# Optimization experiments

Measured on AMD Instinct MI355X. Metric: run time of the kernel, lower is better.

The kernel has to match this reference:

```python
import jax, jax.numpy as jnp
import numpy as np

TEMP = 0.1
EPS = 1e-12  # F.normalize eps


def setup_inputs() -> dict:
    key = jax.random.key(0)
    k1, k2 = jax.random.split(key)
    B, C, N = 8, 128, 4096
    features = jax.random.normal(k1, (B, C, N), dtype=jnp.float32)
    labels_all = jax.random.randint(k2, (B, N), 0, 16, dtype=jnp.int32)
    return {"features": features, "labels_all": labels_all}


def _per_cloud_loss(features_map, labels):
    # features_map: [C, N], labels: [N]
    v = features_map.T  # [N, C]
    v = v / jnp.maximum(jnp.linalg.norm(v, axis=1, keepdims=True), EPS)
    dp = jnp.exp(jnp.matmul(v, v.T) / TEMP)  # [N, N]
    n = dp.shape[0]
    # remove diagonal (dot_products - diag(diagonal))
    dp = dp * (1.0 - jnp.eye(n, dtype=dp.dtype))
    mask = labels[:, None] == labels[None, :]  # [N, N]
    positives = jnp.sum(jnp.where(mask, dp, 0.0), axis=1)
    negatives = jnp.sum(jnp.where(mask, 0.0, dp), axis=1)
    deviation = -jnp.log(positives / (positives + negatives))
    return jnp.mean(deviation)


def reference(features, labels_all):
    # features: [B, C, N], labels_all: [B, N]
    losses = jax.vmap(_per_cloud_loss)(features, labels_all)  # [B]
    return jnp.mean(losses)
```

## Files before the change

kernel.cpp:

```cpp
#include <hip/hip_runtime.h>
#include <hip/hip_bf16.h>
#include <math.h>

#define BATCH 8
#define NPTS 4096
#define CH 128
#define TILE 128

#define SQRT_TEMP_LOG2E 3.79828256f

typedef __attribute__((ext_vector_type(4))) float f32x4;
typedef __attribute__((ext_vector_type(4))) int   i32x4;
typedef __attribute__((ext_vector_type(8))) short bf16x8;

typedef __attribute__((address_space(3))) unsigned int lds_uint;
typedef __attribute__((address_space(1))) const unsigned int gbl_uint;

__device__ __forceinline__ void load_lds16(const void* g, const void* l) {
    __builtin_amdgcn_global_load_lds((gbl_uint*)g, (lds_uint*)l, 16, 0, 0);
}

__device__ __forceinline__ float fast_exp2(float x) {
    return __builtin_amdgcn_exp2f(x);
}

__global__ __launch_bounds__(256) void normalize_kernel(
    const float* __restrict__ f, __hip_bfloat16* __restrict__ vn,
    float* __restrict__ pos, float* __restrict__ neg)
{
    int idx = blockIdx.x * 256 + threadIdx.x;
    int point = idx >> 2, q = idx & 3;
    int b = point >> 12, n = point & (NPTS - 1);
    const float* base = f + (size_t)b * CH * NPTS + (size_t)(q * 32) * NPTS + n;

    float x[32];
    float ss = 0.0f;
    #pragma unroll
    for (int c = 0; c < 32; c++) {
        x[c] = base[(size_t)c * NPTS];
        ss += x[c] * x[c];
    }
    ss += __shfl_xor(ss, 1);
    ss += __shfl_xor(ss, 2);
    float scale = SQRT_TEMP_LOG2E / fmaxf(sqrtf(ss), 1e-12f);

    __hip_bfloat16* out = vn + (size_t)point * CH + q * 32;
    #pragma unroll
    for (int c0 = 0; c0 < 32; c0 += 8) {
        union { __hip_bfloat16 h[8]; uint4 u; } pk;
        #pragma unroll
        for (int j = 0; j < 8; j++)
            pk.h[j] = __float2bfloat16(x[c0 + j] * scale);
        *((uint4*)(out + c0)) = pk.u;
    }
    if (q == 0) pos[point] = 0.0f;
    else if (q == 1) neg[point] = 0.0f;
}

__global__ __launch_bounds__(512, 6) void tile_kernel(
    const __hip_bfloat16* __restrict__ vn, const int* __restrict__ labels,
    float* __restrict__ pos, float* __restrict__ neg)
{
    __shared__ short lB[TILE * CH];
    __shared__ int labC[TILE];

    const int b  = blockIdx.z;
    const int rt = blockIdx.y, ct = blockIdx.x;
    const bool diag = (rt == ct);

    const int tid = threadIdx.x;
    const int w = tid >> 6, lane = tid & 63;
    const int lane15 = lane & 15, quad = lane >> 4;

    const int row0 = rt * TILE, col0 = ct * TILE;
    const __hip_bfloat16* vb = vn + (size_t)b * NPTS * CH;

    if (tid < 128) labC[tid] = labels[b * NPTS + col0 + tid];

    {
        const __hip_bfloat16* Bb = vb + (size_t)col0 * CH;
        #pragma unroll
        for (int i = 0; i < 4; i++) {
            int rsw = (i * 4 + quad) & 15;
            int g   = lane15 ^ rsw;
            int row = w * 16 + i * 4 + quad;
            int ldsrow = w * 16 + i * 4;
            load_lds16(Bb + (size_t)row * CH + g * 8, &lB[ldsrow * CH]);
        }
    }

    const int rowi = w * 16 + lane15;
    bf16x8 afrag[4];
    {
        const __hip_bfloat16* Arow = vb + (size_t)(row0 + rowi) * CH;
        #pragma unroll
        for (int ks = 0; ks < 4; ks++)
            afrag[ks] = *(const bf16x8*)(Arow + (ks * 4 + quad) * 8);
    }
    const int lr = labels[b * NPTS + row0 + rowi];

    __syncthreads();

    f32x4 acc[8] = {};
    #pragma unroll
    for (int ks = 0; ks < 4; ks++) {
        int chunk = ((ks * 4 + quad) ^ lane15) << 3;
        #pragma unroll
        for (int ni = 0; ni < 8; ni++) {
            bf16x8 bfrag = *(const bf16x8*)&lB[(ni * 16 + lane15) * CH + chunk];
            acc[ni] = __builtin_amdgcn_mfma_f32_16x16x32_bf16(
                bfrag, afrag[ks], acc[ni], 0, 0, 0);
        }
    }

    float p = 0.0f, tt = 0.0f;
    if (diag) {
        #pragma unroll
        for (int ni = 0; ni < 8; ni++) {
            const i32x4 lc = *(const i32x4*)&labC[ni * 16 + quad * 4];
            const int jb = ni * 16 + quad * 4;
            #pragma unroll
            for (int r = 0; r < 4; r++) {
                float e = fast_exp2(acc[ni][r]);
                if (rowi == jb + r) e = 0.0f;
                tt += e;
                p  += (lc[r] == lr) ? e : 0.0f;
            }
        }
    } else {
        #pragma unroll
        for (int ni = 0; ni < 8; ni++) {
            const i32x4 lc = *(const i32x4*)&labC[ni * 16 + quad * 4];
            #pragma unroll
            for (int r = 0; r < 4; r++) {
                float e = fast_exp2(acc[ni][r]);
                tt += e;
                p  += (lc[r] == lr) ? e : 0.0f;
            }
        }
    }

    p  += __shfl_xor(p, 16);   p  += __shfl_xor(p, 32);
    tt += __shfl_xor(tt, 16);  tt += __shfl_xor(tt, 32);

    if (lane < 16) {
        atomicAdd(&pos[b * NPTS + row0 + rowi], p);
        atomicAdd(&neg[b * NPTS + row0 + rowi], tt - p);
    }
}

__global__ __launch_bounds__(1024) void finalize_kernel(
    const float* __restrict__ pos, const float* __restrict__ neg,
    float* __restrict__ out)
{
    float acc = 0.0f;
    for (int i = threadIdx.x; i < BATCH * NPTS; i += 1024) {
        float p = pos[i];
        float t = p + neg[i];
        acc += __logf(t / p);
    }
    #pragma unroll
    for (int off = 32; off; off >>= 1) acc += __shfl_down(acc, off);
    __shared__ float red[16];
    if ((threadIdx.x & 63) == 0) red[threadIdx.x >> 6] = acc;
    __syncthreads();
    if (threadIdx.x < 16) {
        float v = red[threadIdx.x];
        #pragma unroll
        for (int off = 8; off; off >>= 1) v += __shfl_down(v, off);
        if (threadIdx.x == 0) out[0] = v * (1.0f / (BATCH * NPTS));
    }
}

extern "C" void kernel_launch(void* const* d_in, const int* in_sizes, int n_in,
                              void* d_out, int out_size, void* d_ws, size_t ws_size,
                              hipStream_t stream)
{
    const float* features = (const float*)d_in[0];
    const int*   labels   = (const int*)d_in[1];
    float*       out      = (float*)d_out;

    __hip_bfloat16* vn = (__hip_bfloat16*)d_ws;
    float* pos = (float*)((char*)d_ws + (size_t)BATCH * NPTS * CH * sizeof(__hip_bfloat16));
    float* neg = pos + BATCH * NPTS;

    hipLaunchKernelGGL(normalize_kernel, dim3(BATCH * NPTS * 4 / 256), dim3(256), 0, stream,
                       features, vn, pos, neg);
    hipLaunchKernelGGL(tile_kernel, dim3(NPTS / TILE, NPTS / TILE, BATCH), dim3(512), 0, stream,
                       vn, labels, pos, neg);
    hipLaunchKernelGGL(finalize_kernel, dim3(1), dim3(1024), 0, stream, pos, neg, out);
}
```

Before: 136.9 us.

## Use 32x32 MFMA with 256-row tiles and fuse finalize via last-block counter

The tile kernel now covers 256 rows per block with 32x32x16 bf16 MFMA instead of 16x16x32, halving the number of blocks and doubling reuse of each LDS-staged column tile. The separate finalize kernel is removed: a global counter, zeroed in the normalize kernel, lets the last finishing tile block compute the log-sum reduction, which saves a kernel launch. Occupancy hint drops from 6 to 4 blocks per CU to fit more registers. The cost is a threadfence and atomic per block, plus a serial tail reduction run by a single block.

```diff
diff --git a/kernel.cpp b/kernel.cpp
--- a/kernel.cpp
+++ b/kernel.cpp
@@ -5,13 +5,13 @@
 #define BATCH 8
 #define NPTS 4096
 #define CH 128
-#define TILE 128
+#define NTILEBLOCKS (32 * 16 * BATCH)
 
 #define SQRT_TEMP_LOG2E 3.79828256f
 
-typedef __attribute__((ext_vector_type(4))) float f32x4;
-typedef __attribute__((ext_vector_type(4))) int   i32x4;
-typedef __attribute__((ext_vector_type(8))) short bf16x8;
+typedef __attribute__((ext_vector_type(16))) float f32x16;
+typedef __attribute__((ext_vector_type(4)))  int   i32x4;
+typedef __attribute__((ext_vector_type(8)))  short bf16x8;
 
 typedef __attribute__((address_space(3))) unsigned int lds_uint;
 typedef __attribute__((address_space(1))) const unsigned int gbl_uint;
@@ -26,7 +26,7 @@
 
 __global__ __launch_bounds__(256) void normalize_kernel(
     const float* __restrict__ f, __hip_bfloat16* __restrict__ vn,
-    float* __restrict__ pos, float* __restrict__ neg)
+    float* __restrict__ pos, float* __restrict__ neg, int* __restrict__ counter)
 {
     int idx = blockIdx.x * 256 + threadIdx.x;
     int point = idx >> 2, q = idx & 3;
@@ -55,24 +55,29 @@
     }
     if (q == 0) pos[point] = 0.0f;
     else if (q == 1) neg[point] = 0.0f;
-}
-
-__global__ __launch_bounds__(512, 6) void tile_kernel(
+    if (idx == 0) *counter = 0;
+}
+
+__global__ __launch_bounds__(512, 4) void tile_kernel(
     const __hip_bfloat16* __restrict__ vn, const int* __restrict__ labels,
-    float* __restrict__ pos, float* __restrict__ neg)
+    float* __restrict__ pos, float* __restrict__ neg,
+    int* __restrict__ counter, float* __restrict__ out)
 {
-    __shared__ short lB[TILE * CH];
-    __shared__ int labC[TILE];
-
-    const int b  = blockIdx.z;
-    const int rt = blockIdx.y, ct = blockIdx.x;
-    const bool diag = (rt == ct);
+    __shared__ short lB[128 * CH];
+    __shared__ int labC[128];
+    __shared__ int lastFlag;
+    __shared__ float red[8];
+
+    const int b   = blockIdx.z;
+    const int ct  = blockIdx.x;
+    const int row0 = blockIdx.y * 256;
+    const int col0 = ct * 128;
 
     const int tid = threadIdx.x;
     const int w = tid >> 6, lane = tid & 63;
-    const int lane15 = lane & 15, quad = lane >> 4;
-
-    const int row0 = rt * TILE, col0 = ct * TILE;
+    const int lane31 = lane & 31, lane15 = lane & 15;
+    const int quad = (lane >> 4) & 3, h = lane >> 5;
+
     const __hip_bfloat16* vb = vn + (size_t)b * NPTS * CH;
 
     if (tid < 128) labC[tid] = labels[b * NPTS + col0 + tid];
@@ -89,86 +94,92 @@
         }
     }
 
-    const int rowi = w * 16 + lane15;
-    bf16x8 afrag[4];
+    const int rowl = w * 32 + lane31;
+    bf16x8 afrag[8];
     {
-        const __hip_bfloat16* Arow = vb + (size_t)(row0 + rowi) * CH;
-        #pragma unroll
-        for (int ks = 0; ks < 4; ks++)
-            afrag[ks] = *(const bf16x8*)(Arow + (ks * 4 + quad) * 8);
-    }
-    const int lr = labels[b * NPTS + row0 + rowi];
+        const __hip_bfloat16* Arow = vb + (size_t)(row0 + rowl) * CH + h * 8;
+        #pragma unroll
+        for (int ks = 0; ks < 8; ks++)
+            afrag[ks] = *(const bf16x8*)(Arow + ks * 16);
+    }
+    const int lr = labels[b * NPTS + row0 + rowl];
 
     __syncthreads();
 
-    f32x4 acc[8] = {};
-    #pragma unroll
-    for (int ks = 0; ks < 4; ks++) {
-        int chunk = ((ks * 4 + quad) ^ lane15) << 3;
-        #pragma unroll
-        for (int ni = 0; ni < 8; ni++) {
-            bf16x8 bfrag = *(const bf16x8*)&lB[(ni * 16 + lane15) * CH + chunk];
-            acc[ni] = __builtin_amdgcn_mfma_f32_16x16x32_bf16(
-                bfrag, afrag[ks], acc[ni], 0, 0, 0);
+    f32x16 acc[4] = {};
+    #pragma unroll
+    for (int ks = 0; ks < 8; ks++) {
+        const int koff = ((2 * ks + h) ^ lane15) << 3;
+        #pragma unroll
+        for (int nb = 0; nb < 4; nb++) {
+            bf16x8 bf = *(const bf16x8*)&lB[(nb * 32 + lane31) * CH + koff];
+            acc[nb] = __builtin_amdgcn_mfma_f32_32x32x16_bf16(
+                bf, afrag[ks], acc[nb], 0, 0, 0);
         }
     }
 
     float p = 0.0f, tt = 0.0f;
-    if (diag) {
-        #pragma unroll
-        for (int ni = 0; ni < 8; ni++) {
-            const i32x4 lc = *(const i32x4*)&labC[ni * 16 + quad * 4];
-            const int jb = ni * 16 + quad * 4;
+    #pragma unroll
+    for (int nb = 0; nb < 4; nb++) {
+        if (row0 + w * 32 == col0 + nb * 32) {
             #pragma unroll
-            for (int r = 0; r < 4; r++) {
-                float e = fast_exp2(acc[ni][r]);
-                if (rowi == jb + r) e = 0.0f;
-                tt += e;
-                p  += (lc[r] == lr) ? e : 0.0f;
+            for (int g = 0; g < 4; g++) {
+                const i32x4 lc = *(const i32x4*)&labC[nb * 32 + g * 8 + 4 * h];
+                #pragma unroll
+                for (int r = 0; r < 4; r++) {
+                    float e = fast_exp2(acc[nb][g * 4 + r]);
+                    if (lane31 == g * 8 + 4 * h + r) e = 0.0f;
+                    tt += e;
+                    p  += (lc[r] == lr) ? e : 0.0f;
+                }
             }
-        }
-    } else {
-        #pragma unroll
-        for (int ni = 0; ni < 8; ni++) {
-            const i32x4 lc = *(const i32x4*)&labC[ni * 16 + quad * 4];
+        } else {
             #pragma unroll
-            for (int r = 0; r < 4; r++) {
-                float e = fast_exp2(acc[ni][r]);
-                tt += e;
-                p  += (lc[r] == lr) ? e : 0.0f;
+            for (int g = 0; g < 4; g++) {
+                const i32x4 lc = *(const i32x4*)&labC[nb * 32 + g * 8 + 4 * h];
+                #pragma unroll
+                for (int r = 0; r < 4; r++) {
+                    float e = fast_exp2(acc[nb][g * 4 + r]);
+                    tt += e;
+                    p  += (lc[r] == lr) ? e : 0.0f;
+                }
             }
         }
     }
 
-    p  += __shfl_xor(p, 16);   p  += __shfl_xor(p, 32);
-    tt += __shfl_xor(tt, 16);  tt += __shfl_xor(tt, 32);
-
-    if (lane < 16) {
-        atomicAdd(&pos[b * NPTS + row0 + rowi], p);
-        atomicAdd(&neg[b * NPTS + row0 + rowi], tt - p);
-    }
-}
-
-__global__ __launch_bounds__(1024) void finalize_kernel(
-    const float* __restrict__ pos, const float* __restrict__ neg,
-    float* __restrict__ out)
-{
-    float acc = 0.0f;
-    for (int i = threadIdx.x; i < BATCH * NPTS; i += 1024) {
-        float p = pos[i];
-        float t = p + neg[i];
-        acc += __logf(t / p);
-    }
-    #pragma unroll
-    for (int off = 32; off; off >>= 1) acc += __shfl_down(acc, off);
-    __shared__ float red[16];
-    if ((threadIdx.x & 63) == 0) red[threadIdx.x >> 6] = acc;
+    p  += __shfl_xor(p, 32);
+    tt += __shfl_xor(tt, 32);
+    if (lane < 32) {
+        atomicAdd(&pos[b * NPTS + row0 + rowl], p);
+        atomicAdd(&neg[b * NPTS + row0 + rowl], tt - p);
+    }
+
     __syncthreads();
-    if (threadIdx.x < 16) {
-        float v = red[threadIdx.x];
-        #pragma unroll
-        for (int off = 8; off; off >>= 1) v += __shfl_down(v, off);
-        if (threadIdx.x == 0) out[0] = v * (1.0f / (BATCH * NPTS));
+    if (tid == 0) {
+        __threadfence();
+        int c = atomicAdd(counter, 1);
+        lastFlag = (c == NTILEBLOCKS - 1);
+    }
+    __syncthreads();
+    if (lastFlag) {
+        __threadfence();
+        volatile const float* vp = pos;
+        volatile const float* vq = neg;
+        float acc2 = 0.0f;
+        for (int i = tid; i < BATCH * NPTS; i += 512) {
+            float pp = vp[i], qq = vq[i];
+            acc2 += __logf((pp + qq) / pp);
+        }
+        #pragma unroll
+        for (int off = 32; off; off >>= 1) acc2 += __shfl_down(acc2, off);
+        if (lane == 0) red[w] = acc2;
+        __syncthreads();
+        if (tid < 8) {
+            float v = red[tid];
+            #pragma unroll
+            for (int off = 4; off; off >>= 1) v += __shfl_down(v, off);
+            if (tid == 0) out[0] = v * (1.0f / (BATCH * NPTS));
+        }
     }
 }
 
@@ -183,10 +194,10 @@
     __hip_bfloat16* vn = (__hip_bfloat16*)d_ws;
     float* pos = (float*)((char*)d_ws + (size_t)BATCH * NPTS * CH * sizeof(__hip_bfloat16));
     float* neg = pos + BATCH * NPTS;
+    int* counter = (int*)(neg + BATCH * NPTS);
 
     hipLaunchKernelGGL(normalize_kernel, dim3(BATCH * NPTS * 4 / 256), dim3(256), 0, stream,
-                       features, vn, pos, neg);
-    hipLaunchKernelGGL(tile_kernel, dim3(NPTS / TILE, NPTS / TILE, BATCH), dim3(512), 0, stream,
-                       vn, labels, pos, neg);
-    hipLaunchKernelGGL(finalize_kernel, dim3(1), dim3(1024), 0, stream, pos, neg, out);
-}
+                       features, vn, pos, neg, counter);
+    hipLaunchKernelGGL(tile_kernel, dim3(32, 16, BATCH), dim3(512), 0, stream,
+                       vn, labels, pos, neg, counter, out);
+}
```

New measurement: 220.6 us. +61.1%, slower.
